# Kernel optimization log

Hardware: AMD Instinct MI355X
Metric: run time of the kernel (lower is better)

## Reference

```python
import jax, jax.numpy as jnp
import numpy as np

B, T, DIN, D = 32, 2048, 512, 512


def setup_inputs() -> dict:
    key = jax.random.key(0)
    k0, k1, k2, k3 = jax.random.split(key, 4)
    x = jax.random.normal(k0, (B, T, DIN), dtype=jnp.float32)
    h0 = jax.random.normal(k1, (B, D), dtype=jnp.float32)
    s0 = jax.random.normal(k2, (B, D), dtype=jnp.float32)
    # nn.Linear(input_dim, 6*hidden_dim): weight [6D, DIN], bias [6D]
    W = jax.random.normal(k3, (6 * D, DIN), dtype=jnp.float32) / np.float32(np.sqrt(DIN))
    b = jnp.zeros((6 * D,), dtype=jnp.float32)
    return {"x": x, "h0": h0, "s0": s0, "W": W, "b": b}


def reference(x, h0, s0, W, b):
    # Fused input projection for all 6 gates, done once as a big GEMM: [B,T,6D]
    proj = jnp.einsum("bti,oi->bto", x, W) + b
    proj = jnp.transpose(proj, (1, 0, 2))  # [T, B, 6D] for scan over time
    sig = jax.nn.sigmoid

    def step(carry, z):
        h, s = carry  # each [B, D]
        z0, z1, z2, z3, z4, z5 = jnp.split(z, 6, axis=-1)
        # gated two-state recurrence (6 gates, input-only projection,
        # elementwise recurrence on h/s as in the fused Triton cell)
        s_new = sig(z0) * s + sig(z1) * jnp.tanh(z2)
        h_new = sig(z3) * h + sig(z4) * jnp.tanh(z5 + s_new)
        return (h_new, s_new), h_new

    (hT, sT), hs = jax.lax.scan(step, (h0, s0), proj)
    out = jnp.transpose(hs, (1, 0, 2))  # [B, T, D]
    return out, sT
```

## Files before the change

kernel.cpp:

```cpp
#include <hip/hip_runtime.h>
#include <hip/hip_bf16.h>
#include <cstddef>
#include <cstdint>

#define BB   32
#define TT   2048
#define DIN  512
#define DD   512
#define NN   3072
#define PW   3072
#define PF   16

#define BMT 256
#define BNT 256
#define BKT 64
#define NKT (DIN / BKT)

typedef __attribute__((ext_vector_type(4))) float f32x4;
typedef __attribute__((ext_vector_type(8))) short s16x8;

__device__ __forceinline__ void gl2lds16(const void* g, void* l) {
    __builtin_amdgcn_global_load_lds(
        (const __attribute__((address_space(1))) unsigned*)g,
        (__attribute__((address_space(3))) unsigned*)l, 16, 0, 0);
}

__device__ __forceinline__ unsigned short bfr(float f) {
    unsigned u = __float_as_uint(f);
    u += 0x7fffu + ((u >> 16) & 1u);
    return (unsigned short)(u >> 16);
}

__device__ __forceinline__ float ftanh(float x) {
    return 1.f - 2.f * __builtin_amdgcn_rcpf(1.f + __builtin_amdgcn_exp2f(x * 2.885390082f));
}

__device__ __forceinline__ float h2lo(unsigned u) {
    return (float)__builtin_bit_cast(_Float16, (unsigned short)(u & 0xffffu));
}
__device__ __forceinline__ float h2hi(unsigned u) {
    return (float)__builtin_bit_cast(_Float16, (unsigned short)(u >> 16));
}

__global__ __launch_bounds__(256) void convert_x(
    const float* __restrict__ x, unsigned short* __restrict__ x2)
{
    const int total4 = BB * TT * DIN / 4;
    for (int idx = blockIdx.x * 256 + threadIdx.x; idx < total4;
         idx += gridDim.x * 256) {
        int e = idx * 4;
        int b = e >> 20;
        int t = (e >> 9) & 2047;
        int i = e & 511;
        float4 v = *(const float4*)(x + (size_t)e);
        ushort4 o;
        o.x = bfr(v.x); o.y = bfr(v.y); o.z = bfr(v.z); o.w = bfr(v.w);
        *(ushort4*)(x2 + ((size_t)((t << 5) | b) << 9) + i) = o;
    }
}

__global__ __launch_bounds__(128) void convert_w(
    const float* __restrict__ W, const float* __restrict__ bias,
    unsigned short* __restrict__ W2, float* __restrict__ bias2)
{
    int c = blockIdx.x;
    int p = c >> 10, d = (c & 1023) >> 1, q = c & 1;
    int o = ((2 * p + q) << 9) + d;
    const float* src = W + (size_t)o * DIN;
    unsigned short* dst = W2 + (size_t)c * DIN;
    int i = threadIdx.x * 4;
    float4 v = *(const float4*)(src + i);
    ushort4 u;
    u.x = bfr(v.x); u.y = bfr(v.y); u.z = bfr(v.z); u.w = bfr(v.w);
    *(ushort4*)(dst + i) = u;
    if (threadIdx.x == 0) bias2[c] = bias[o];
}

__global__ __launch_bounds__(512, 2) void gemm_proj8(
    const unsigned short* __restrict__ x2,
    const unsigned short* __restrict__ W2,
    const float* __restrict__ bias2,
    _Float16* __restrict__ proj,
    int t0)
{
    __shared__ unsigned short lds[4 * 256 * 64];
    unsigned short* const Abuf[2] = { lds,          lds + 32768 };
    unsigned short* const Bbuf[2] = { lds + 16384,  lds + 49152 };

    const unsigned nwg = gridDim.x;
    const unsigned fb  = blockIdx.x;
    const unsigned qq  = nwg >> 3, rr8 = nwg & 7;
    const unsigned xcd = fb & 7, sid = fb >> 3;
    const unsigned work = (xcd < rr8 ? xcd * (qq + 1)
                                     : rr8 * (qq + 1) + (xcd - rr8) * qq) + sid;
    const int bx = (int)(work % (NN / BNT));
    const int by = (int)(work / (NN / BNT));

    const int tid  = threadIdx.x;
    const int row0 = by * BMT;
    const int col0 = bx * BNT;
    const size_t growA = (size_t)t0 * BB + row0;

    const int lane = tid & 63;
    const int wv   = tid >> 6;
    const int wm   = wv >> 2;
    const int wn   = wv & 3;
    const int lr   = lane & 15;
    const int lq   = lane >> 4;

    auto stageA = [&](unsigned short* Ab, int kt) {
        const int k0 = kt * BKT;
        #pragma unroll
        for (int a = 0; a < 4; ++a) {
            int cid = a * 512 + tid;
            int rt  = cid >> 3;
            int cp  = cid & 7;
            int cl  = cp ^ (rt & 7);
            gl2lds16(x2 + (growA + rt) * DIN + k0 + cl * 8, Ab + rt * 64 + cp * 8);
        }
    };
    auto stageB = [&](unsigned short* Bb, int kt) {
        const int k0 = kt * BKT;
        #pragma unroll
        for (int a = 0; a < 4; ++a) {
            int cid = a * 512 + tid;
            int rt  = cid >> 3;
            int cp  = cid & 7;
            int cl  = cp ^ (rt & 7);
            gl2lds16(W2 + (size_t)(col0 + rt) * DIN + k0 + cl * 8, Bb + rt * 64 + cp * 8);
        }
    };

    f32x4 acc[8][4] = {};

    stageA(Abuf[0], 0); stageB(Bbuf[0], 0);
    stageA(Abuf[1], 1); stageB(Bbuf[1], 1);
    asm volatile("s_waitcnt vmcnt(8)" ::: "memory");
    __builtin_amdgcn_s_barrier();

    #pragma unroll
    for (int kt = 0; kt < NKT; ++kt) {
        const unsigned short* Ab = Abuf[kt & 1];
        const unsigned short* Bb = Bbuf[kt & 1];

        s16x8 bv[4][2];
        #pragma unroll
        for (int j = 0; j < 4; ++j) {
            int col = wn * 64 + j * 16 + lr;
            #pragma unroll
            for (int x = 0; x < 2; ++x) {
                int cp = (x * 4 + lq) ^ (col & 7);
                bv[j][x] = *(const s16x8*)(Bb + col * 64 + cp * 8);
            }
        }
        asm volatile("s_waitcnt lgkmcnt(0)" ::: "memory");
        __builtin_amdgcn_sched_barrier(0);
        __builtin_amdgcn_s_barrier();
        if (kt + 2 < NKT) stageB(Bbuf[kt & 1], kt + 2);

        #pragma unroll
        for (int m = 0; m < 8; ++m) {
            int row = wm * 128 + m * 16 + lr;
            int cp0 = (lq)     ^ (row & 7);
            int cp1 = (4 + lq) ^ (row & 7);
            s16x8 av0 = *(const s16x8*)(Ab + row * 64 + cp0 * 8);
            s16x8 av1 = *(const s16x8*)(Ab + row * 64 + cp1 * 8);
            __builtin_amdgcn_s_setprio(1);
            #pragma unroll
            for (int j = 0; j < 4; ++j) {
                acc[m][j] = __builtin_amdgcn_mfma_f32_16x16x32_bf16(
                    bv[j][0], av0, acc[m][j], 0, 0, 0);
                acc[m][j] = __builtin_amdgcn_mfma_f32_16x16x32_bf16(
                    bv[j][1], av1, acc[m][j], 0, 0, 0);
            }
            __builtin_amdgcn_s_setprio(0);
        }
        asm volatile("s_waitcnt lgkmcnt(0)" ::: "memory");
        __builtin_amdgcn_sched_barrier(0);
        __builtin_amdgcn_s_barrier();

        if (kt + 2 < NKT) {
            stageA(Abuf[kt & 1], kt + 2);
            asm volatile("s_waitcnt vmcnt(8)" ::: "memory");
        } else if (kt + 1 < NKT) {
            asm volatile("s_waitcnt vmcnt(0)" ::: "memory");
        }
        if (kt + 1 < NKT) __builtin_amdgcn_s_barrier();
    }

    const int p = col0 >> 10;
    const bool evenTanh = (p == 1);
    const bool oddIdent = (p == 2);
    const float mEven = evenTanh ? 2.885390082f : -1.442695041f;

    #pragma unroll
    for (int m = 0; m < 8; ++m) {
        int prow = row0 + wm * 128 + m * 16 + lr;
        _Float16* dst = proj + (size_t)prow * PW;
        #pragma unroll
        for (int j = 0; j < 4; ++j) {
            int cbase = col0 + wn * 64 + j * 16 + lq * 4;
            float4 bc = *(const float4*)(bias2 + cbase);
            float z0 = acc[m][j][0] + bc.x;
            float z1 = acc[m][j][1] + bc.y;
            float z2 = acc[m][j][2] + bc.z;
            float z3 = acc[m][j][3] + bc.w;
            float e0 = __builtin_amdgcn_rcpf(1.f + __builtin_amdgcn_exp2f(z0 * mEven));
            float e2 = __builtin_amdgcn_rcpf(1.f + __builtin_amdgcn_exp2f(z2 * mEven));
            float v0 = evenTanh ? (1.f - 2.f * e0) : e0;
            float v2 = evenTanh ? (1.f - 2.f * e2) : e2;
            float v1 = oddIdent ? z1
                : __builtin_amdgcn_rcpf(1.f + __builtin_amdgcn_exp2f(z1 * -1.442695041f));
            float v3 = oddIdent ? z3
                : __builtin_amdgcn_rcpf(1.f + __builtin_amdgcn_exp2f(z3 * -1.442695041f));
            ushort4 o;
            o.x = __builtin_bit_cast(unsigned short, (_Float16)v0);
            o.y = __builtin_bit_cast(unsigned short, (_Float16)v1);
            o.z = __builtin_bit_cast(unsigned short, (_Float16)v2);
            o.w = __builtin_bit_cast(unsigned short, (_Float16)v3);
            *(ushort4*)(dst + cbase) = o;
        }
    }
}

__global__ __launch_bounds__(64) void scan_chunk(
    const _Float16* __restrict__ proj,
    const float* __restrict__ h0, const float* __restrict__ s0,
    float* __restrict__ outH, float* __restrict__ outS,
    int t0, int Tc)
{
    const int gid = blockIdx.x * 64 + threadIdx.x;
    const int b   = gid >> 9;
    const int d   = gid & 511;

    float h, s;
    if (t0 == 0) { h = h0[gid]; s = s0[gid]; }
    else {
        h = outH[((size_t)b * TT + (t0 - 1)) * DD + d];
        s = outS[gid];
    }

    const unsigned* pu = (const unsigned*)(proj + (size_t)b * PW + d * 2);
    const size_t tstr = (size_t)BB * PW / 2;
    float* oH = outH + ((size_t)b * TT + t0) * DD + d;

    unsigned bufA[PF][3], bufB[PF][3];
    #pragma unroll
    for (int u = 0; u < PF; ++u)
        #pragma unroll
        for (int p = 0; p < 3; ++p)
            bufA[u][p] = pu[(size_t)u * tstr + p * 512];

    for (int tb = 0; tb < Tc; tb += 2 * PF) {
        #pragma unroll
        for (int u = 0; u < PF; ++u) {
            int t = tb + PF + u; if (t > Tc - 1) t = Tc - 1;
            #pragma unroll
            for (int p = 0; p < 3; ++p)
                bufB[u][p] = pu[(size_t)t * tstr + p * 512];
        }
        #pragma unroll
        for (int u = 0; u < PF; ++u) {
            float a0 = h2lo(bufA[u][0]), a1 = h2hi(bufA[u][0]);
            float t2 = h2lo(bufA[u][1]), a3 = h2hi(bufA[u][1]);
            float a4 = h2lo(bufA[u][2]), z5 = h2hi(bufA[u][2]);
            s = __builtin_fmaf(a0, s, a1 * t2);
            h = __builtin_fmaf(a3, h, a4 * ftanh(z5 + s));
            oH[(size_t)(tb + u) * DD] = h;
        }
        #pragma unroll
        for (int u = 0; u < PF; ++u) {
            int t = tb + 2 * PF + u; if (t > Tc - 1) t = Tc - 1;
            #pragma unroll
            for (int p = 0; p < 3; ++p)
                bufA[u][p] = pu[(size_t)t * tstr + p * 512];
        }
        #pragma unroll
        for (int u = 0; u < PF; ++u) {
            float a0 = h2lo(bufB[u][0]), a1 = h2hi(bufB[u][0]);
            float t2 = h2lo(bufB[u][1]), a3 = h2hi(bufB[u][1]);
            float a4 = h2lo(bufB[u][2]), z5 = h2hi(bufB[u][2]);
            s = __builtin_fmaf(a0, s, a1 * t2);
            h = __builtin_fmaf(a3, h, a4 * ftanh(z5 + s));
            oH[(size_t)(tb + PF + u) * DD] = h;
        }
    }

    outS[gid] = s;
}

extern "C" void kernel_launch(void* const* d_in, const int* in_sizes, int n_in,
                              void* d_out, int out_size, void* d_ws, size_t ws_size,
                              hipStream_t stream) {
    const float* x    = (const float*)d_in[0];
    const float* h0   = (const float*)d_in[1];
    const float* s0   = (const float*)d_in[2];
    const float* W    = (const float*)d_in[3];
    const float* bias = (const float*)d_in[4];

    float* outH = (float*)d_out;
    float* outS = outH + (size_t)BB * TT * DD;

    char* ws = (char*)d_ws;
    const size_t x2_bytes = (size_t)BB * TT * DIN * 2;
    const size_t w2_bytes = (size_t)NN * DIN * 2;
    const size_t b2_bytes = (size_t)NN * 4;
    unsigned short* x2    = (unsigned short*)ws;
    unsigned short* W2    = (unsigned short*)(ws + x2_bytes);
    float*          bias2 = (float*)(ws + x2_bytes + w2_bytes);
    _Float16*       proj  = (_Float16*)(ws + x2_bytes + w2_bytes + b2_bytes);

    const size_t fixed = x2_bytes + w2_bytes + b2_bytes;
    const size_t per_t = (size_t)BB * PW * 2;
    size_t avail = ws_size > fixed ? ws_size - fixed : 0;
    int TcMax = (int)(avail / per_t);
    if (TcMax > 512) TcMax = 512;
    TcMax &= ~31;
    if (TcMax < 32) TcMax = 32;

    convert_x<<<2048, 256, 0, stream>>>(x, x2);
    convert_w<<<NN, 128, 0, stream>>>(W, bias, W2, bias2);

    for (int t0 = 0; t0 < TT; t0 += TcMax) {
        int Tc = TT - t0;
        if (Tc > TcMax) Tc = TcMax;
        int nblk = (NN / BNT) * (Tc * BB / BMT);
        gemm_proj8<<<nblk, 512, 0, stream>>>(x2, W2, bias2, proj, t0);
        scan_chunk<<<(BB * DD) / 64, 64, 0, stream>>>(proj, h0, s0, outH, outS, t0, Tc);
    }
}
```

Baseline: 492.1 us.

## Pre-tile x into MFMA fragment layout and load A operands directly from global

The x conversion kernel now writes bf16 data in a blocked layout (16-row by 8-k fragments) that matches the MFMA A-operand register layout. The GEMM no longer stages A through LDS. Each wave reads its A fragments straight from global memory into registers, and only B stays double-buffered in LDS. This removes half the LDS traffic and one barrier per k-step, in exchange for redundant global/L2 reads of A across the 4 wn-waves and the 12 column blocks, plus global load latency that is no longer hidden by prefetch.

```diff
diff --git a/kernel.cpp b/kernel.cpp
--- a/kernel.cpp
+++ b/kernel.cpp
@@ -43,19 +43,25 @@
 }
 
 __global__ __launch_bounds__(256) void convert_x(
-    const float* __restrict__ x, unsigned short* __restrict__ x2)
+    const float* __restrict__ x, unsigned short* __restrict__ x3)
 {
-    const int total4 = BB * TT * DIN / 4;
-    for (int idx = blockIdx.x * 256 + threadIdx.x; idx < total4;
+    const int total8 = BB * TT * DIN / 8;
+    for (int idx = blockIdx.x * 256 + threadIdx.x; idx < total8;
          idx += gridDim.x * 256) {
-        int e = idx * 4;
+        int e = idx * 8;
         int b = e >> 20;
         int t = (e >> 9) & 2047;
         int i = e & 511;
-        float4 v = *(const float4*)(x + (size_t)e);
-        ushort4 o;
-        o.x = bfr(v.x); o.y = bfr(v.y); o.z = bfr(v.z); o.w = bfr(v.w);
-        *(ushort4*)(x2 + ((size_t)((t << 5) | b) << 9) + i) = o;
+        float4 v0 = *(const float4*)(x + (size_t)e);
+        float4 v1 = *(const float4*)(x + (size_t)e + 4);
+        int r    = (t << 5) | b;
+        int rblk = r >> 4, lr = r & 15;
+        int kblk = i >> 3;
+        unsigned short o[8];
+        o[0] = bfr(v0.x); o[1] = bfr(v0.y); o[2] = bfr(v0.z); o[3] = bfr(v0.w);
+        o[4] = bfr(v1.x); o[5] = bfr(v1.y); o[6] = bfr(v1.z); o[7] = bfr(v1.w);
+        *(uint4*)(x3 + (size_t)rblk * 8192 + kblk * 128 + lr * 8) =
+            *(const uint4*)o;
     }
 }
 
@@ -76,16 +82,14 @@
     if (threadIdx.x == 0) bias2[c] = bias[o];
 }
 
-__global__ __launch_bounds__(512, 2) void gemm_proj8(
-    const unsigned short* __restrict__ x2,
+__global__ __launch_bounds__(512, 2) void gemm_proj9(
+    const unsigned short* __restrict__ x3,
     const unsigned short* __restrict__ W2,
     const float* __restrict__ bias2,
     _Float16* __restrict__ proj,
     int t0)
 {
-    __shared__ unsigned short lds[4 * 256 * 64];
-    unsigned short* const Abuf[2] = { lds,          lds + 32768 };
-    unsigned short* const Bbuf[2] = { lds + 16384,  lds + 49152 };
+    __shared__ unsigned short Bs[2][256 * 64];
 
     const unsigned nwg = gridDim.x;
     const unsigned fb  = blockIdx.x;
@@ -99,7 +103,6 @@
     const int tid  = threadIdx.x;
     const int row0 = by * BMT;
     const int col0 = bx * BNT;
-    const size_t growA = (size_t)t0 * BB + row0;
 
     const int lane = tid & 63;
     const int wv   = tid >> 6;
@@ -108,17 +111,10 @@
     const int lr   = lane & 15;
     const int lq   = lane >> 4;
 
-    auto stageA = [&](unsigned short* Ab, int kt) {
-        const int k0 = kt * BKT;
-        #pragma unroll
-        for (int a = 0; a < 4; ++a) {
-            int cid = a * 512 + tid;
-            int rt  = cid >> 3;
-            int cp  = cid & 7;
-            int cl  = cp ^ (rt & 7);
-            gl2lds16(x2 + (growA + rt) * DIN + k0 + cl * 8, Ab + rt * 64 + cp * 8);
-        }
-    };
+    const int rblk0 = ((t0 << 5) + row0) >> 4;
+    const unsigned short* pA =
+        x3 + (size_t)(rblk0 + wm * 8) * 8192 + lq * 128 + lr * 8;
+
     auto stageB = [&](unsigned short* Bb, int kt) {
         const int k0 = kt * BKT;
         #pragma unroll
@@ -133,15 +129,21 @@
 
     f32x4 acc[8][4] = {};
 
-    stageA(Abuf[0], 0); stageB(Bbuf[0], 0);
-    stageA(Abuf[1], 1); stageB(Bbuf[1], 1);
-    asm volatile("s_waitcnt vmcnt(8)" ::: "memory");
+    stageB(Bs[0], 0);
+    stageB(Bs[1], 1);
+    asm volatile("s_waitcnt vmcnt(4)" ::: "memory");
     __builtin_amdgcn_s_barrier();
 
     #pragma unroll
     for (int kt = 0; kt < NKT; ++kt) {
-        const unsigned short* Ab = Abuf[kt & 1];
-        const unsigned short* Bb = Bbuf[kt & 1];
+        const unsigned short* Bb = Bs[kt & 1];
+
+        s16x8 av[8][2];
+        #pragma unroll
+        for (int m = 0; m < 8; ++m)
+            #pragma unroll
+            for (int x = 0; x < 2; ++x)
+                av[m][x] = *(const s16x8*)(pA + m * 8192 + kt * 1024 + x * 512);
 
         s16x8 bv[4][2];
         #pragma unroll
@@ -156,36 +158,28 @@
         asm volatile("s_waitcnt lgkmcnt(0)" ::: "memory");
         __builtin_amdgcn_sched_barrier(0);
         __builtin_amdgcn_s_barrier();
-        if (kt + 2 < NKT) stageB(Bbuf[kt & 1], kt + 2);
+        if (kt + 2 < NKT) stageB(Bs[kt & 1], kt + 2);
 
         #pragma unroll
         for (int m = 0; m < 8; ++m) {
-            int row = wm * 128 + m * 16 + lr;
-            int cp0 = (lq)     ^ (row & 7);
-            int cp1 = (4 + lq) ^ (row & 7);
-            s16x8 av0 = *(const s16x8*)(Ab + row * 64 + cp0 * 8);
-            s16x8 av1 = *(const s16x8*)(Ab + row * 64 + cp1 * 8);
             __builtin_amdgcn_s_setprio(1);
             #pragma unroll
             for (int j = 0; j < 4; ++j) {
                 acc[m][j] = __builtin_amdgcn_mfma_f32_16x16x32_bf16(
-                    bv[j][0], av0, acc[m][j], 0, 0, 0);
+                    bv[j][0], av[m][0], acc[m][j], 0, 0, 0);
                 acc[m][j] = __builtin_amdgcn_mfma_f32_16x16x32_bf16(
-                    bv[j][1], av1, acc[m][j], 0, 0, 0);
+                    bv[j][1], av[m][1], acc[m][j], 0, 0, 0);
             }
             __builtin_amdgcn_s_setprio(0);
         }
-        asm volatile("s_waitcnt lgkmcnt(0)" ::: "memory");
-        __builtin_amdgcn_sched_barrier(0);
-        __builtin_amdgcn_s_barrier();
-
-        if (kt + 2 < NKT) {
-            stageA(Abuf[kt & 1], kt + 2);
-            asm volatile("s_waitcnt vmcnt(8)" ::: "memory");
-        } else if (kt + 1 < NKT) {
-            asm volatile("s_waitcnt vmcnt(0)" ::: "memory");
-        }
-        if (kt + 1 < NKT) __builtin_amdgcn_s_barrier();
+
+        if (kt + 1 < NKT) {
+            if (kt + 2 < NKT)
+                asm volatile("s_waitcnt vmcnt(4)" ::: "memory");
+            else
+                asm volatile("s_waitcnt vmcnt(0)" ::: "memory");
+            __builtin_amdgcn_s_barrier();
+        }
     }
 
     const int p = col0 >> 10;
@@ -302,15 +296,15 @@
     float* outS = outH + (size_t)BB * TT * DD;
 
     char* ws = (char*)d_ws;
-    const size_t x2_bytes = (size_t)BB * TT * DIN * 2;
+    const size_t x3_bytes = (size_t)BB * TT * DIN * 2;
     const size_t w2_bytes = (size_t)NN * DIN * 2;
     const size_t b2_bytes = (size_t)NN * 4;
-    unsigned short* x2    = (unsigned short*)ws;
-    unsigned short* W2    = (unsigned short*)(ws + x2_bytes);
-    float*          bias2 = (float*)(ws + x2_bytes + w2_bytes);
-    _Float16*       proj  = (_Float16*)(ws + x2_bytes + w2_bytes + b2_bytes);
-
-    const size_t fixed = x2_bytes + w2_bytes + b2_bytes;
+    unsigned short* x3    = (unsigned short*)ws;
+    unsigned short* W2    = (unsigned short*)(ws + x3_bytes);
+    float*          bias2 = (float*)(ws + x3_bytes + w2_bytes);
+    _Float16*       proj  = (_Float16*)(ws + x3_bytes + w2_bytes + b2_bytes);
+
+    const size_t fixed = x3_bytes + w2_bytes + b2_bytes;
     const size_t per_t = (size_t)BB * PW * 2;
     size_t avail = ws_size > fixed ? ws_size - fixed : 0;
     int TcMax = (int)(avail / per_t);
@@ -318,14 +312,14 @@
     TcMax &= ~31;
     if (TcMax < 32) TcMax = 32;
 
-    convert_x<<<2048, 256, 0, stream>>>(x, x2);
+    convert_x<<<2048, 256, 0, stream>>>(x, x3);
     convert_w<<<NN, 128, 0, stream>>>(W, bias, W2, bias2);
 
     for (int t0 = 0; t0 < TT; t0 += TcMax) {
         int Tc = TT - t0;
         if (Tc > TcMax) Tc = TcMax;
         int nblk = (NN / BNT) * (Tc * BB / BMT);
-        gemm_proj8<<<nblk, 512, 0, stream>>>(x2, W2, bias2, proj, t0);
+        gemm_proj9<<<nblk, 512, 0, stream>>>(x3, W2, bias2, proj, t0);
         scan_chunk<<<(BB * DD) / 64, 64, 0, stream>>>(proj, h0, s0, outH, outS, t0, Tc);
     }
 }
```

Result: slower. 673.0 us (+36.7%).

## Use triple-buffered LDS with K-tile 32 and one barrier per iteration

Applied to the files above, without the earlier changes.

The GEMM's K-tile shrinks from 64 to 32 and the two LDS buffers become three, so loads for tile kt+2 are issued at the top of each iteration and only one barrier per step is needed instead of three. The XOR swizzle on LDS rows is dropped, and all A/B fragments are loaded before one block of MFMAs. This cuts synchronisation and LDS footprint (96KB to 96KB→48KB-equivalent per stage layout) at the cost of twice as many iterations and possible LDS bank conflicts from the unswizzled 64-byte row stride.

```diff
diff --git a/kernel.cpp b/kernel.cpp
--- a/kernel.cpp
+++ b/kernel.cpp
@@ -13,7 +13,7 @@
 
 #define BMT 256
 #define BNT 256
-#define BKT 64
+#define BKT 32
 #define NKT (DIN / BKT)
 
 typedef __attribute__((ext_vector_type(4))) float f32x4;
@@ -76,16 +76,14 @@
     if (threadIdx.x == 0) bias2[c] = bias[o];
 }
 
-__global__ __launch_bounds__(512, 2) void gemm_proj8(
+__global__ __launch_bounds__(512, 2) void gemm_proj10(
     const unsigned short* __restrict__ x2,
     const unsigned short* __restrict__ W2,
     const float* __restrict__ bias2,
     _Float16* __restrict__ proj,
     int t0)
 {
-    __shared__ unsigned short lds[4 * 256 * 64];
-    unsigned short* const Abuf[2] = { lds,          lds + 32768 };
-    unsigned short* const Bbuf[2] = { lds + 16384,  lds + 49152 };
+    __shared__ unsigned short lds[3 * 16384];
 
     const unsigned nwg = gridDim.x;
     const unsigned fb  = blockIdx.x;
@@ -108,84 +106,71 @@
     const int lr   = lane & 15;
     const int lq   = lane >> 4;
 
-    auto stageA = [&](unsigned short* Ab, int kt) {
+    auto stageA = [&](int s, int kt) {
+        unsigned short* Ab = lds + s * 16384;
         const int k0 = kt * BKT;
         #pragma unroll
-        for (int a = 0; a < 4; ++a) {
+        for (int a = 0; a < 2; ++a) {
             int cid = a * 512 + tid;
-            int rt  = cid >> 3;
-            int cp  = cid & 7;
-            int cl  = cp ^ (rt & 7);
-            gl2lds16(x2 + (growA + rt) * DIN + k0 + cl * 8, Ab + rt * 64 + cp * 8);
+            int rt  = cid >> 2;
+            int cp  = cid & 3;
+            gl2lds16(x2 + (growA + rt) * DIN + k0 + cp * 8, Ab + cid * 8);
         }
     };
-    auto stageB = [&](unsigned short* Bb, int kt) {
+    auto stageB = [&](int s, int kt) {
+        unsigned short* Bb = lds + s * 16384 + 8192;
         const int k0 = kt * BKT;
         #pragma unroll
-        for (int a = 0; a < 4; ++a) {
+        for (int a = 0; a < 2; ++a) {
             int cid = a * 512 + tid;
-            int rt  = cid >> 3;
-            int cp  = cid & 7;
-            int cl  = cp ^ (rt & 7);
-            gl2lds16(W2 + (size_t)(col0 + rt) * DIN + k0 + cl * 8, Bb + rt * 64 + cp * 8);
+            int rt  = cid >> 2;
+            int cp  = cid & 3;
+            gl2lds16(W2 + (size_t)(col0 + rt) * DIN + k0 + cp * 8, Bb + cid * 8);
         }
     };
 
     f32x4 acc[8][4] = {};
 
-    stageA(Abuf[0], 0); stageB(Bbuf[0], 0);
-    stageA(Abuf[1], 1); stageB(Bbuf[1], 1);
-    asm volatile("s_waitcnt vmcnt(8)" ::: "memory");
+    stageA(0, 0); stageB(0, 0);
+    stageA(1, 1); stageB(1, 1);
+    asm volatile("s_waitcnt vmcnt(4)" ::: "memory");
     __builtin_amdgcn_s_barrier();
 
     #pragma unroll
     for (int kt = 0; kt < NKT; ++kt) {
-        const unsigned short* Ab = Abuf[kt & 1];
-        const unsigned short* Bb = Bbuf[kt & 1];
-
-        s16x8 bv[4][2];
+        const unsigned short* Ab = lds + (kt % 3) * 16384;
+        const unsigned short* Bb = Ab + 8192;
+        const int  ks = (kt + 2) % 3;
+        const bool st = (kt + 2) < NKT;
+
+        if (st) { stageA(ks, kt + 2); stageB(ks, kt + 2); }
+
+        s16x8 bv[4], av[8];
         #pragma unroll
         for (int j = 0; j < 4; ++j) {
             int col = wn * 64 + j * 16 + lr;
-            #pragma unroll
-            for (int x = 0; x < 2; ++x) {
-                int cp = (x * 4 + lq) ^ (col & 7);
-                bv[j][x] = *(const s16x8*)(Bb + col * 64 + cp * 8);
-            }
-        }
-        asm volatile("s_waitcnt lgkmcnt(0)" ::: "memory");
-        __builtin_amdgcn_sched_barrier(0);
-        __builtin_amdgcn_s_barrier();
-        if (kt + 2 < NKT) stageB(Bbuf[kt & 1], kt + 2);
-
+            bv[j] = *(const s16x8*)(Bb + col * BKT + lq * 8);
+        }
         #pragma unroll
         for (int m = 0; m < 8; ++m) {
             int row = wm * 128 + m * 16 + lr;
-            int cp0 = (lq)     ^ (row & 7);
-            int cp1 = (4 + lq) ^ (row & 7);
-            s16x8 av0 = *(const s16x8*)(Ab + row * 64 + cp0 * 8);
-            s16x8 av1 = *(const s16x8*)(Ab + row * 64 + cp1 * 8);
-            __builtin_amdgcn_s_setprio(1);
+            av[m] = *(const s16x8*)(Ab + row * BKT + lq * 8);
+        }
+
+        __builtin_amdgcn_s_setprio(1);
+        #pragma unroll
+        for (int m = 0; m < 8; ++m)
             #pragma unroll
-            for (int j = 0; j < 4; ++j) {
+            for (int j = 0; j < 4; ++j)
                 acc[m][j] = __builtin_amdgcn_mfma_f32_16x16x32_bf16(
-                    bv[j][0], av0, acc[m][j], 0, 0, 0);
-                acc[m][j] = __builtin_amdgcn_mfma_f32_16x16x32_bf16(
-                    bv[j][1], av1, acc[m][j], 0, 0, 0);
-            }
-            __builtin_amdgcn_s_setprio(0);
-        }
-        asm volatile("s_waitcnt lgkmcnt(0)" ::: "memory");
-        __builtin_amdgcn_sched_barrier(0);
-        __builtin_amdgcn_s_barrier();
-
-        if (kt + 2 < NKT) {
-            stageA(Abuf[kt & 1], kt + 2);
-            asm volatile("s_waitcnt vmcnt(8)" ::: "memory");
-        } else if (kt + 1 < NKT) {
-            asm volatile("s_waitcnt vmcnt(0)" ::: "memory");
-        }
-        if (kt + 1 < NKT) __builtin_amdgcn_s_barrier();
+                    bv[j], av[m], acc[m][j], 0, 0, 0);
+        __builtin_amdgcn_s_setprio(0);
+
+        if (kt + 1 < NKT) {
+            if (st) asm volatile("s_waitcnt vmcnt(4)" ::: "memory");
+            else    asm volatile("s_waitcnt vmcnt(0)" ::: "memory");
+            __builtin_amdgcn_s_barrier();
+        }
     }
 
     const int p = col0 >> 10;
@@ -325,7 +310,7 @@
         int Tc = TT - t0;
         if (Tc > TcMax) Tc = TcMax;
         int nblk = (NN / BNT) * (Tc * BB / BMT);
-        gemm_proj8<<<nblk, 512, 0, stream>>>(x2, W2, bias2, proj, t0);
+        gemm_proj10<<<nblk, 512, 0, stream>>>(x2, W2, bias2, proj, t0);
         scan_chunk<<<(BB * DD) / 64, 64, 0, stream>>>(proj, h0, s0, outH, outS, t0, Tc);
     }
 }
```

Measured after the change: 487.8 us. About the same (-0.9%).
